# Kernel optimization log

Hardware: AMD Instinct MI355X
Metric: run time of the kernel (lower is better)

The kernel has to match this reference:

```python
import jax, jax.numpy as jnp
import numpy as np

N_NODES = 100000
N_EDGES = 1600000
D_IN, D_HID, D_OUT = 64, 64, 32


def setup_inputs() -> dict:
    key = jax.random.key(0)
    ks = jax.random.split(key, 9)
    x = jax.random.normal(ks[0], (N_NODES, D_IN), dtype=jnp.float32)
    edge_index = jax.random.randint(ks[1], (2, N_EDGES), 0, N_NODES, dtype=jnp.int64)
    s1 = 1.0 / np.sqrt(D_IN)
    s2 = 1.0 / np.sqrt(D_HID)
    return {
        "x": x,
        "edge_index": edge_index,
        # layer 1: lin_l (aggregated neighbors, has bias), lin_r (root, no bias)
        "W1_l": jax.random.uniform(ks[2], (D_IN, D_HID), jnp.float32, -s1, s1),
        "b1": jax.random.uniform(ks[3], (D_HID,), jnp.float32, -s1, s1),
        "W1_r": jax.random.uniform(ks[4], (D_IN, D_HID), jnp.float32, -s1, s1),
        # layer 2
        "W2_l": jax.random.uniform(ks[5], (D_HID, D_OUT), jnp.float32, -s2, s2),
        "b2": jax.random.uniform(ks[6], (D_OUT,), jnp.float32, -s2, s2),
        "W2_r": jax.random.uniform(ks[7], (D_HID, D_OUT), jnp.float32, -s2, s2),
    }


def _sage_conv(x, src, dst, W_l, b_l, W_r, n_nodes):
    """PyG SAGEConv with mean aggregation:
       out_i = W_l @ mean_{j in N(i)} x_j + b_l + W_r @ x_i
    """
    msgs = x[src]  # [E, d] gather of source-node features
    summed = jax.ops.segment_sum(msgs, dst, num_segments=n_nodes)  # [N, d]
    deg = jax.ops.segment_sum(jnp.ones((src.shape[0],), x.dtype), dst, num_segments=n_nodes)
    mean = summed / jnp.maximum(deg, 1.0)[:, None]
    return mean @ W_l + b_l + x @ W_r


def reference(x, edge_index, W1_l, b1, W1_r, W2_l, b2, W2_r):
    src, dst = edge_index[0], edge_index[1]
    n = x.shape[0]
    h = _sage_conv(x, src, dst, W1_l, b1, W1_r, n)
    h = jax.nn.relu(h)
    out = _sage_conv(h, src, dst, W2_l, b2, W2_r, n)
    return out
```

## Files before the change

### kernel.cpp

```cpp
#include <hip/hip_runtime.h>


typedef __attribute__((ext_vector_type(4))) float f4;
typedef __attribute__((ext_vector_type(2))) float f2;
typedef __attribute__((ext_vector_type(4))) unsigned short us4;
typedef __attribute__((ext_vector_type(8))) unsigned short us8;
typedef __attribute__((ext_vector_type(8))) short bfrag;

#define BSHIFT 9
#define BSZ (1 << BSHIFT)
#define NBMAX 256
#define NBLK 512
#define LSTR 72

static __device__ inline unsigned short f2bf(float f) {
    union { float f; unsigned u; } v; v.f = f;
    unsigned u = v.u;
    u = (u + 0x7FFFu + ((u >> 16) & 1u)) >> 16;
    return (unsigned short)u;
}
static __device__ inline float bf2f(unsigned short h) {
    union { unsigned u; float f; } v; v.u = ((unsigned)h) << 16; return v.f;
}

__global__ __launch_bounds__(256) void k_g1h(const float* __restrict__ x,
                                             const float* __restrict__ Wl,
                                             const float* __restrict__ Wr, int N, int gb,
                                             unsigned char* __restrict__ t1l8,
                                             unsigned short* __restrict__ t1rb,
                                             const int* __restrict__ dst, int E, int chunk,
                                             int NB, int* __restrict__ cntmat) {
    __shared__ unsigned short smem[64 * LSTR + 128 * LSTR];
    int t = threadIdx.x;
    if ((int)blockIdx.x >= gb) {
        int* hist = (int*)smem;
        hist[t] = 0;
        __syncthreads();
        int bb = blockIdx.x - gb;
        int lo = bb * chunk, hi = min(lo + chunk, E);
        for (int e = lo + t; e < hi; e += 256) atomicAdd(&hist[dst[e] >> BSHIFT], 1);
        __syncthreads();
        if (t < NB) cntmat[bb * NB + t] = hist[t];
        return;
    }
    unsigned short* sX = smem;
    unsigned short* sW = smem + 64 * LSTR;
    int r0 = blockIdx.x * 64;
    for (int i = t; i < 2048; i += 256) {
        int which = i >> 10;
        int rem = i & 1023;
        int k = rem >> 4;
        int c4 = (rem & 15) * 4;
        f4 v = *(const f4*)&(which ? Wr : Wl)[k * 64 + c4];
        int nb = which * 64 + c4;
        sW[(nb + 0) * LSTR + k] = f2bf(v[0]);
        sW[(nb + 1) * LSTR + k] = f2bf(v[1]);
        sW[(nb + 2) * LSTR + k] = f2bf(v[2]);
        sW[(nb + 3) * LSTR + k] = f2bf(v[3]);
    }
    {
        int row = t >> 2;
        int q = (t & 3) * 16;
        bool valid = (r0 + row) < N;
#pragma unroll
        for (int j = 0; j < 4; j++) {
            f4 v = {0.f, 0.f, 0.f, 0.f};
            if (valid) v = *(const f4*)&x[(size_t)(r0 + row) * 64 + q + j * 4];
            us4 bv;
            bv[0] = f2bf(v[0]); bv[1] = f2bf(v[1]); bv[2] = f2bf(v[2]); bv[3] = f2bf(v[3]);
            *(us4*)&sX[row * LSTR + q + j * 4] = bv;
        }
    }
    __syncthreads();
    int wv = t >> 6;
    int l  = t & 63;
    int lm = l & 15;
    int lk = (l >> 4) * 8;
    f4 acc[8] = {{0.f,0.f,0.f,0.f},{0.f,0.f,0.f,0.f},{0.f,0.f,0.f,0.f},{0.f,0.f,0.f,0.f},
                 {0.f,0.f,0.f,0.f},{0.f,0.f,0.f,0.f},{0.f,0.f,0.f,0.f},{0.f,0.f,0.f,0.f}};
#pragma unroll
    for (int kh = 0; kh < 2; kh++) {
        bfrag a = *(const bfrag*)&sX[(wv * 16 + lm) * LSTR + kh * 32 + lk];
#pragma unroll
        for (int nt = 0; nt < 8; nt++) {
            bfrag b = *(const bfrag*)&sW[(nt * 16 + lm) * LSTR + kh * 32 + lk];
            acc[nt] = __builtin_amdgcn_mfma_f32_16x16x32_bf16(a, b, acc[nt], 0, 0, 0);
        }
    }
    int orow0 = r0 + wv * 16 + (l >> 4) * 4;
#pragma unroll
    for (int j = 0; j < 4; j++) {
        int rr = orow0 + j;
        if (rr < N) {
#pragma unroll
            for (int nt = 0; nt < 4; nt++) {
                float v = acc[nt][j];
                unsigned w8 = __builtin_amdgcn_cvt_pk_fp8_f32(v, v, 0u, false);
                t1l8[(size_t)rr * 64 + nt * 16 + lm] = (unsigned char)(w8 & 0xFFu);
            }
#pragma unroll
            for (int nt = 0; nt < 4; nt++) {
                t1rb[(size_t)rr * 64 + nt * 16 + lm] = f2bf(acc[nt + 4][j]);
            }
        }
    }
}

__global__ __launch_bounds__(256) void k_cscan(int* __restrict__ cntmat, int NB, int E, int N,
                                               int* __restrict__ btot, int* __restrict__ row_off) {
    __shared__ int wt[4];
    int b = blockIdx.x;
    int t = threadIdx.x;
    int v0 = cntmat[(2 * t) * NB + b];
    int v1 = cntmat[(2 * t + 1) * NB + b];
    int tsum = v0 + v1;
    int lane = t & 63, w = t >> 6;
    int p = tsum;
    for (int off = 1; off < 64; off <<= 1) { int u = __shfl_up(p, off); if (lane >= off) p += u; }
    if (lane == 63) wt[w] = p;
    __syncthreads();
    int wb = 0;
    for (int i = 0; i < w; i++) wb += wt[i];
    int excl = wb + p - tsum;
    cntmat[(2 * t) * NB + b] = excl;
    cntmat[(2 * t + 1) * NB + b] = excl + v0;
    if (t == 255) btot[b] = wb + p;
    if (b == 0 && t == 0) row_off[N] = E;
}

__global__ __launch_bounds__(256) void k_bscatter(const int* __restrict__ src, const int* __restrict__ dst,
                                                  int E, int chunk, int NB,
                                                  const int* __restrict__ btot,
                                                  const int* __restrict__ cntmat,
                                                  unsigned int* __restrict__ bdata) {
    __shared__ int lbase[NBMAX], lcur[NBMAX];
    __shared__ int wt[4];
    int t = threadIdx.x;
    int v = (t < NB) ? btot[t] : 0;
    int lane = t & 63, w = t >> 6;
    int p = v;
    for (int off = 1; off < 64; off <<= 1) { int u = __shfl_up(p, off); if (lane >= off) p += u; }
    if (lane == 63) wt[w] = p;
    __syncthreads();
    int wb = 0;
    for (int i = 0; i < w; i++) wb += wt[i];
    int excl = wb + p - v;
    if (t < NB) { lbase[t] = excl + cntmat[blockIdx.x * NB + t]; lcur[t] = 0; }
    __syncthreads();
    int lo = blockIdx.x * chunk, hi = min(lo + chunk, E);
    for (int e = lo + t; e < hi; e += 256) {
        int d = dst[e];
        int b = d >> BSHIFT;
        int pos = lbase[b] + atomicAdd(&lcur[b], 1);
        bdata[pos] = ((unsigned)(d & (BSZ - 1)) << 17) | (unsigned)src[e];
    }
}

__global__ __launch_bounds__(256) void k_bucket_csr(const unsigned int* __restrict__ bdata,
                                                    const int* __restrict__ btot, int NB,
                                                    int N, int* __restrict__ row_off,
                                                    int* __restrict__ col_src) {
    __shared__ int fh[BSZ];
    __shared__ int wt1[4], wt2[4];
    __shared__ int sb[2];
    int t = threadIdx.x;
    int b = blockIdx.x;
    {
        int v = (t < NB) ? btot[t] : 0;
        int lane = t & 63, w = t >> 6;
        int p = v;
        for (int off = 1; off < 64; off <<= 1) { int u = __shfl_up(p, off); if (lane >= off) p += u; }
        if (lane == 63) wt1[w] = p;
        __syncthreads();
        int wb = 0;
        for (int i = 0; i < w; i++) wb += wt1[i];
        int excl = wb + p - v;
        if (t == b) { sb[0] = excl; sb[1] = excl + v; }
    }
    fh[2 * t] = 0; fh[2 * t + 1] = 0;
    __syncthreads();
    int ebase = sb[0], eend = sb[1];
    for (int i = ebase + t; i < eend; i += 256) atomicAdd(&fh[bdata[i] >> 17], 1);
    __syncthreads();
    int a0 = fh[2 * t], a1 = fh[2 * t + 1];
    int psum = a0 + a1;
    int lane = t & 63, w = t >> 6;
    int v = psum;
    for (int off = 1; off < 64; off <<= 1) { int u = __shfl_up(v, off); if (lane >= off) v += u; }
    if (lane == 63) wt2[w] = v;
    __syncthreads();
    int wbase = 0;
    for (int i = 0; i < w; i++) wbase += wt2[i];
    int excl = wbase + v - psum;
    int e0 = excl, e1 = excl + a0;
    int n0 = (b << BSHIFT) + 2 * t, n1 = n0 + 1;
    if (n0 < N) row_off[n0] = ebase + e0;
    if (n1 < N) row_off[n1] = ebase + e1;
    fh[2 * t] = e0; fh[2 * t + 1] = e1;
    __syncthreads();
    for (int i = ebase + t; i < eend; i += 256) {
        unsigned vv = bdata[i];
        int dl = vv >> 17;
        int pos = atomicAdd(&fh[dl], 1);
        col_src[ebase + pos] = (int)(vv & 0x1FFFFu);
    }
}

__global__ __launch_bounds__(256) void k_gemm2(const unsigned short* __restrict__ hbf,
                                               const float* __restrict__ Wl,
                                               const float* __restrict__ Wr,
                                               const float* __restrict__ b2, int N,
                                               unsigned short* __restrict__ t2l,
                                               float* __restrict__ t2r) {
    __shared__ unsigned short sX[64 * LSTR];
    __shared__ unsigned short sW[64 * LSTR];
    int t = threadIdx.x;
    int r0 = blockIdx.x * 64;
    for (int i = t; i < 1024; i += 256) {
        int which = i >> 9;
        int rem = i & 511;
        int k = rem >> 3;
        int c4 = (rem & 7) * 4;
        f4 v = *(const f4*)&(which ? Wr : Wl)[k * 32 + c4];
        int nb = which * 32 + c4;
        sW[(nb + 0) * LSTR + k] = f2bf(v[0]);
        sW[(nb + 1) * LSTR + k] = f2bf(v[1]);
        sW[(nb + 2) * LSTR + k] = f2bf(v[2]);
        sW[(nb + 3) * LSTR + k] = f2bf(v[3]);
    }
    {
        int row = t >> 2;
        int q = (t & 3) * 16;
        us8 z = {0,0,0,0,0,0,0,0};
        us8 v0 = z, v1 = z;
        if (r0 + row < N) {
            v0 = *(const us8*)&hbf[(size_t)(r0 + row) * 64 + q];
            v1 = *(const us8*)&hbf[(size_t)(r0 + row) * 64 + q + 8];
        }
        *(us8*)&sX[row * LSTR + q] = v0;
        *(us8*)&sX[row * LSTR + q + 8] = v1;
    }
    __syncthreads();
    int wv = t >> 6;
    int l  = t & 63;
    int lm = l & 15;
    int lk = (l >> 4) * 8;
    f4 acc[4] = {{0.f,0.f,0.f,0.f},{0.f,0.f,0.f,0.f},{0.f,0.f,0.f,0.f},{0.f,0.f,0.f,0.f}};
#pragma unroll
    for (int kh = 0; kh < 2; kh++) {
        bfrag a = *(const bfrag*)&sX[(wv * 16 + lm) * LSTR + kh * 32 + lk];
#pragma unroll
        for (int nt = 0; nt < 4; nt++) {
            bfrag b = *(const bfrag*)&sW[(nt * 16 + lm) * LSTR + kh * 32 + lk];
            acc[nt] = __builtin_amdgcn_mfma_f32_16x16x32_bf16(a, b, acc[nt], 0, 0, 0);
        }
    }
    int orow0 = r0 + wv * 16 + (l >> 4) * 4;
#pragma unroll
    for (int j = 0; j < 4; j++) {
        int rr = orow0 + j;
        if (rr < N) {
#pragma unroll
            for (int nt = 0; nt < 2; nt++) {
                t2l[(size_t)rr * 32 + nt * 16 + lm] = f2bf(acc[nt][j]);
            }
#pragma unroll
            for (int nt = 0; nt < 2; nt++) {
                int c = nt * 16 + lm;
                t2r[(size_t)rr * 32 + c] = acc[nt + 2][j] + b2[c];
            }
        }
    }
}

__global__ __launch_bounds__(256) void k_agg1(const unsigned char* __restrict__ t1l8,
                                              const int* __restrict__ row_off,
                                              const int* __restrict__ col_src,
                                              const float* __restrict__ b1,
                                              const unsigned short* __restrict__ t1rb,
                                              int N, unsigned short* __restrict__ hbf) {
    int gid = (blockIdx.x * blockDim.x + threadIdx.x) >> 4;
    int gl  = threadIdx.x & 15;
    if (gid >= N) return;
    int beg = row_off[gid], end = row_off[gid + 1];
    f4 a0 = {0.f,0.f,0.f,0.f}, a1 = {0.f,0.f,0.f,0.f};
    f4 a2 = {0.f,0.f,0.f,0.f}, a3 = {0.f,0.f,0.f,0.f};
    int k = beg;
    for (; k + 7 < end; k += 8) {
        int i0 = col_src[k],     i1 = col_src[k + 1], i2 = col_src[k + 2], i3 = col_src[k + 3];
        int i4 = col_src[k + 4], i5 = col_src[k + 5], i6 = col_src[k + 6], i7 = col_src[k + 7];
        unsigned u0 = *(const unsigned*)&t1l8[(size_t)i0 * 64 + gl * 4];
        unsigned u1 = *(const unsigned*)&t1l8[(size_t)i1 * 64 + gl * 4];
        unsigned u2 = *(const unsigned*)&t1l8[(size_t)i2 * 64 + gl * 4];
        unsigned u3 = *(const unsigned*)&t1l8[(size_t)i3 * 64 + gl * 4];
        unsigned u4 = *(const unsigned*)&t1l8[(size_t)i4 * 64 + gl * 4];
        unsigned u5 = *(const unsigned*)&t1l8[(size_t)i5 * 64 + gl * 4];
        unsigned u6 = *(const unsigned*)&t1l8[(size_t)i6 * 64 + gl * 4];
        unsigned u7 = *(const unsigned*)&t1l8[(size_t)i7 * 64 + gl * 4];
        f2 l0 = __builtin_amdgcn_cvt_pk_f32_fp8(u0, false), h0 = __builtin_amdgcn_cvt_pk_f32_fp8(u0, true);
        f2 l1 = __builtin_amdgcn_cvt_pk_f32_fp8(u1, false), h1 = __builtin_amdgcn_cvt_pk_f32_fp8(u1, true);
        f2 l2 = __builtin_amdgcn_cvt_pk_f32_fp8(u2, false), h2 = __builtin_amdgcn_cvt_pk_f32_fp8(u2, true);
        f2 l3 = __builtin_amdgcn_cvt_pk_f32_fp8(u3, false), h3 = __builtin_amdgcn_cvt_pk_f32_fp8(u3, true);
        f2 l4 = __builtin_amdgcn_cvt_pk_f32_fp8(u4, false), h4 = __builtin_amdgcn_cvt_pk_f32_fp8(u4, true);
        f2 l5 = __builtin_amdgcn_cvt_pk_f32_fp8(u5, false), h5 = __builtin_amdgcn_cvt_pk_f32_fp8(u5, true);
        f2 l6 = __builtin_amdgcn_cvt_pk_f32_fp8(u6, false), h6 = __builtin_amdgcn_cvt_pk_f32_fp8(u6, true);
        f2 l7 = __builtin_amdgcn_cvt_pk_f32_fp8(u7, false), h7 = __builtin_amdgcn_cvt_pk_f32_fp8(u7, true);
        a0[0] += l0[0] + l4[0]; a0[1] += l0[1] + l4[1]; a0[2] += h0[0] + h4[0]; a0[3] += h0[1] + h4[1];
        a1[0] += l1[0] + l5[0]; a1[1] += l1[1] + l5[1]; a1[2] += h1[0] + h5[0]; a1[3] += h1[1] + h5[1];
        a2[0] += l2[0] + l6[0]; a2[1] += l2[1] + l6[1]; a2[2] += h2[0] + h6[0]; a2[3] += h2[1] + h6[1];
        a3[0] += l3[0] + l7[0]; a3[1] += l3[1] + l7[1]; a3[2] += h3[0] + h7[0]; a3[3] += h3[1] + h7[1];
    }
    for (; k + 3 < end; k += 4) {
        int i0 = col_src[k], i1 = col_src[k + 1], i2 = col_src[k + 2], i3 = col_src[k + 3];
        unsigned u0 = *(const unsigned*)&t1l8[(size_t)i0 * 64 + gl * 4];
        unsigned u1 = *(const unsigned*)&t1l8[(size_t)i1 * 64 + gl * 4];
        unsigned u2 = *(const unsigned*)&t1l8[(size_t)i2 * 64 + gl * 4];
        unsigned u3 = *(const unsigned*)&t1l8[(size_t)i3 * 64 + gl * 4];
        f2 l0 = __builtin_amdgcn_cvt_pk_f32_fp8(u0, false), h0 = __builtin_amdgcn_cvt_pk_f32_fp8(u0, true);
        f2 l1 = __builtin_amdgcn_cvt_pk_f32_fp8(u1, false), h1 = __builtin_amdgcn_cvt_pk_f32_fp8(u1, true);
        f2 l2 = __builtin_amdgcn_cvt_pk_f32_fp8(u2, false), h2 = __builtin_amdgcn_cvt_pk_f32_fp8(u2, true);
        f2 l3 = __builtin_amdgcn_cvt_pk_f32_fp8(u3, false), h3 = __builtin_amdgcn_cvt_pk_f32_fp8(u3, true);
        a0[0] += l0[0]; a0[1] += l0[1]; a0[2] += h0[0]; a0[3] += h0[1];
        a1[0] += l1[0]; a1[1] += l1[1]; a1[2] += h1[0]; a1[3] += h1[1];
        a2[0] += l2[0]; a2[1] += l2[1]; a2[2] += h2[0]; a2[3] += h2[1];
        a3[0] += l3[0]; a3[1] += l3[1]; a3[2] += h3[0]; a3[3] += h3[1];
    }
    for (; k < end; k++) {
        unsigned u0 = *(const unsigned*)&t1l8[(size_t)col_src[k] * 64 + gl * 4];
        f2 l0 = __builtin_amdgcn_cvt_pk_f32_fp8(u0, false), h0 = __builtin_amdgcn_cvt_pk_f32_fp8(u0, true);
        a0[0] += l0[0]; a0[1] += l0[1]; a0[2] += h0[0]; a0[3] += h0[1];
    }
    f4 s = (a0 + a1) + (a2 + a3);
    float deg = (float)(end - beg);
    float inv = deg > 0.f ? 1.f / deg : 0.f;
    us4 rb = *(const us4*)&t1rb[(size_t)gid * 64 + gl * 4];
    f4 bb = *(const f4*)&b1[gl * 4];
    us4 ob;
#pragma unroll
    for (int j = 0; j < 4; j++) {
        float v = s[j] * inv + bf2f(rb[j]) + bb[j];
        ob[j] = f2bf(v > 0.f ? v : 0.f);
    }
    *(us4*)&hbf[(size_t)gid * 64 + gl * 4] = ob;
}

__global__ __launch_bounds__(256) void k_agg2(const unsigned short* __restrict__ t2l,
                                              const float* __restrict__ t2r,
                                              const int* __restrict__ row_off,
                                              const int* __restrict__ col_src,
                                              int N, float* __restrict__ out) {
    int gid = (blockIdx.x * blockDim.x + threadIdx.x) >> 4;
    int gl  = threadIdx.x & 15;
    if (gid >= N) return;
    int beg = row_off[gid], end = row_off[gid + 1];
    f2 a0 = {0.f,0.f}, a1 = {0.f,0.f}, a2 = {0.f,0.f}, a3 = {0.f,0.f};
    int k = beg;
    for (; k + 7 < end; k += 8) {
        int i0 = col_src[k],     i1 = col_src[k + 1], i2 = col_src[k + 2], i3 = col_src[k + 3];
        int i4 = col_src[k + 4], i5 = col_src[k + 5], i6 = col_src[k + 6], i7 = col_src[k + 7];
        unsigned u0 = *(const unsigned*)&t2l[(size_t)i0 * 32 + gl * 2];
        unsigned u1 = *(const unsigned*)&t2l[(size_t)i1 * 32 + gl * 2];
        unsigned u2 = *(const unsigned*)&t2l[(size_t)i2 * 32 + gl * 2];
        unsigned u3 = *(const unsigned*)&t2l[(size_t)i3 * 32 + gl * 2];
        unsigned u4 = *(const unsigned*)&t2l[(size_t)i4 * 32 + gl * 2];
        unsigned u5 = *(const unsigned*)&t2l[(size_t)i5 * 32 + gl * 2];
        unsigned u6 = *(const unsigned*)&t2l[(size_t)i6 * 32 + gl * 2];
        unsigned u7 = *(const unsigned*)&t2l[(size_t)i7 * 32 + gl * 2];
        a0[0] += bf2f((unsigned short)(u0 & 0xFFFFu)) + bf2f((unsigned short)(u4 & 0xFFFFu));
        a0[1] += bf2f((unsigned short)(u0 >> 16))     + bf2f((unsigned short)(u4 >> 16));
        a1[0] += bf2f((unsigned short)(u1 & 0xFFFFu)) + bf2f((unsigned short)(u5 & 0xFFFFu));
        a1[1] += bf2f((unsigned short)(u1 >> 16))     + bf2f((unsigned short)(u5 >> 16));
        a2[0] += bf2f((unsigned short)(u2 & 0xFFFFu)) + bf2f((unsigned short)(u6 & 0xFFFFu));
        a2[1] += bf2f((unsigned short)(u2 >> 16))     + bf2f((unsigned short)(u6 >> 16));
        a3[0] += bf2f((unsigned short)(u3 & 0xFFFFu)) + bf2f((unsigned short)(u7 & 0xFFFFu));
        a3[1] += bf2f((unsigned short)(u3 >> 16))     + bf2f((unsigned short)(u7 >> 16));
    }
    for (; k + 3 < end; k += 4) {
        int i0 = col_src[k], i1 = col_src[k + 1], i2 = col_src[k + 2], i3 = col_src[k + 3];
        unsigned u0 = *(const unsigned*)&t2l[(size_t)i0 * 32 + gl * 2];
        unsigned u1 = *(const unsigned*)&t2l[(size_t)i1 * 32 + gl * 2];
        unsigned u2 = *(const unsigned*)&t2l[(size_t)i2 * 32 + gl * 2];
        unsigned u3 = *(const unsigned*)&t2l[(size_t)i3 * 32 + gl * 2];
        a0[0] += bf2f((unsigned short)(u0 & 0xFFFFu)); a0[1] += bf2f((unsigned short)(u0 >> 16));
        a1[0] += bf2f((unsigned short)(u1 & 0xFFFFu)); a1[1] += bf2f((unsigned short)(u1 >> 16));
        a2[0] += bf2f((unsigned short)(u2 & 0xFFFFu)); a2[1] += bf2f((unsigned short)(u2 >> 16));
        a3[0] += bf2f((unsigned short)(u3 & 0xFFFFu)); a3[1] += bf2f((unsigned short)(u3 >> 16));
    }
    for (; k < end; k++) {
        unsigned u0 = *(const unsigned*)&t2l[(size_t)col_src[k] * 32 + gl * 2];
        a0[0] += bf2f((unsigned short)(u0 & 0xFFFFu)); a0[1] += bf2f((unsigned short)(u0 >> 16));
    }
    f2 s = (a0 + a1) + (a2 + a3);
    float deg = (float)(end - beg);
    float inv = deg > 0.f ? 1.f / deg : 0.f;
    f2 rr = *(const f2*)&t2r[(size_t)gid * 32 + gl * 2];
    f2 o = {s[0] * inv + rr[0], s[1] * inv + rr[1]};
    *(f2*)&out[(size_t)gid * 32 + gl * 2] = o;
}

extern "C" void kernel_launch(void* const* d_in, const int* in_sizes, int n_in,
                              void* d_out, int out_size, void* d_ws, size_t ws_size,
                              hipStream_t stream) {
    const float* x   = (const float*)d_in[0];
    const int*   ei  = (const int*)d_in[1];
    const float* W1l = (const float*)d_in[2];
    const float* b1  = (const float*)d_in[3];
    const float* W1r = (const float*)d_in[4];
    const float* W2l = (const float*)d_in[5];
    const float* b2  = (const float*)d_in[6];
    const float* W2r = (const float*)d_in[7];
    float* out = (float*)d_out;

    int N = in_sizes[0] / 64;
    int E = in_sizes[1] / 2;
    const int* src = ei;
    const int* dst = ei + E;
    int NB = (N + BSZ - 1) >> BSHIFT;

    char* ws = (char*)d_ws;
    size_t off = 0;
    auto alloc = [&](size_t bytes) { void* p = ws + off; off += (bytes + 255) & ~(size_t)255; return p; };
    int* cntmat      = (int*)alloc((size_t)NBLK * NB * 4);
    int* btot        = (int*)alloc((size_t)NB * 4);
    int* row_off     = (int*)alloc((size_t)(N + 1) * 4);
    int* col_src     = (int*)alloc((size_t)E * 4);
    unsigned int* bdata = (unsigned int*)alloc((size_t)E * 4);
    unsigned char* t1l8 = (unsigned char*)alloc((size_t)N * 64);
    unsigned short* t1rb = (unsigned short*)alloc((size_t)N * 64 * 2);
    unsigned short* hbf  = (unsigned short*)alloc((size_t)N * 64 * 2);

    unsigned short* t2l = (unsigned short*)bdata;
    float* t2r          = (float*)t1rb;

    int chunk = (E + NBLK - 1) / NBLK;
    int gb = (N + 63) / 64;

    k_g1h<<<gb + NBLK, 256, 0, stream>>>(x, W1l, W1r, N, gb, t1l8, t1rb,
                                         dst, E, chunk, NB, cntmat);
    k_cscan<<<NB, 256, 0, stream>>>(cntmat, NB, E, N, btot, row_off);
    k_bscatter<<<NBLK, 256, 0, stream>>>(src, dst, E, chunk, NB, btot, cntmat, bdata);
    k_bucket_csr<<<NB, 256, 0, stream>>>(bdata, btot, NB, N, row_off, col_src);

    k_agg1<<<((size_t)N * 16 + 255) / 256, 256, 0, stream>>>(t1l8, row_off, col_src, b1, t1rb, N, hbf);
    k_gemm2<<<gb, 256, 0, stream>>>(hbf, W2l, W2r, b2, N, t2l, t2r);
    k_agg2<<<((size_t)N * 16 + 255) / 256, 256, 0, stream>>>(t2l, t2r, row_off, col_src, N, out);
}
```

Measured before the change: 129.5 us.

## Fuse layer-1 aggregation with layer-2 GEMM and LDS-sort bucket scatter

Merges the layer-1 mean aggregation with the layer-2 MFMA GEMM into one kernel. Each 256-thread block aggregates 16 nodes into shared memory, then one wave computes their 16x64 output tile. This removes the hidden-activation round trip through global memory and one kernel launch. The cost is that every block reloads and converts W2 to bf16, and only one wave does the MFMA work. Separately, the bucket scatter now sorts each chunk of edges by bucket in LDS before writing, so global writes to bdata become contiguous runs instead of random stores.

```diff
diff --git a/kernel.cpp b/kernel.cpp
--- a/kernel.cpp
+++ b/kernel.cpp
@@ -11,6 +11,7 @@
 #define BSZ (1 << BSHIFT)
 #define NBMAX 256
 #define NBLK 512
+#define CHMAX 3328
 #define LSTR 72
 
 static __device__ inline unsigned short f2bf(float f) {
@@ -133,26 +134,59 @@
                                                   const int* __restrict__ btot,
                                                   const int* __restrict__ cntmat,
                                                   unsigned int* __restrict__ bdata) {
-    __shared__ int lbase[NBMAX], lcur[NBMAX];
+    __shared__ int lcnt[NBMAX], loff[NBMAX], lcur[NBMAX], gbase[NBMAX];
     __shared__ int wt[4];
+    __shared__ unsigned ldst[CHMAX];
+    __shared__ unsigned srec[CHMAX];
+    __shared__ unsigned char sbk[CHMAX];
     int t = threadIdx.x;
-    int v = (t < NB) ? btot[t] : 0;
-    int lane = t & 63, w = t >> 6;
-    int p = v;
-    for (int off = 1; off < 64; off <<= 1) { int u = __shfl_up(p, off); if (lane >= off) p += u; }
-    if (lane == 63) wt[w] = p;
-    __syncthreads();
-    int wb = 0;
-    for (int i = 0; i < w; i++) wb += wt[i];
-    int excl = wb + p - v;
-    if (t < NB) { lbase[t] = excl + cntmat[blockIdx.x * NB + t]; lcur[t] = 0; }
-    __syncthreads();
-    int lo = blockIdx.x * chunk, hi = min(lo + chunk, E);
-    for (int e = lo + t; e < hi; e += 256) {
-        int d = dst[e];
+    {
+        int v = (t < NB) ? btot[t] : 0;
+        int lane = t & 63, w = t >> 6;
+        int p = v;
+        for (int off = 1; off < 64; off <<= 1) { int u = __shfl_up(p, off); if (lane >= off) p += u; }
+        if (lane == 63) wt[w] = p;
+        __syncthreads();
+        int wb = 0;
+        for (int i = 0; i < w; i++) wb += wt[i];
+        int excl = wb + p - v;
+        if (t < NB) gbase[t] = excl + cntmat[blockIdx.x * NB + t];
+        lcnt[t] = 0;
+    }
+    __syncthreads();
+    int lo = blockIdx.x * chunk;
+    int n = min(chunk, E - lo);
+    for (int i = t; i < n; i += 256) {
+        int d = dst[lo + i];
+        ldst[i] = (unsigned)d;
+        atomicAdd(&lcnt[d >> BSHIFT], 1);
+    }
+    __syncthreads();
+    {
+        int v = lcnt[t];
+        int lane = t & 63, w = t >> 6;
+        int p = v;
+        for (int off = 1; off < 64; off <<= 1) { int u = __shfl_up(p, off); if (lane >= off) p += u; }
+        __syncthreads();
+        if (lane == 63) wt[w] = p;
+        __syncthreads();
+        int wb = 0;
+        for (int i = 0; i < w; i++) wb += wt[i];
+        loff[t] = wb + p - v;
+        lcur[t] = 0;
+    }
+    __syncthreads();
+    for (int i = t; i < n; i += 256) {
+        int d = (int)ldst[i];
         int b = d >> BSHIFT;
-        int pos = lbase[b] + atomicAdd(&lcur[b], 1);
-        bdata[pos] = ((unsigned)(d & (BSZ - 1)) << 17) | (unsigned)src[e];
+        int pos = loff[b] + atomicAdd(&lcur[b], 1);
+        srec[pos] = ((unsigned)(d & (BSZ - 1)) << 17) | (unsigned)src[lo + i];
+        sbk[pos] = (unsigned char)b;
+    }
+    __syncthreads();
+    for (int i = t; i < n; i += 256) {
+        int b = sbk[i];
+        bdata[gbase[b] + (i - loff[b])] = srec[i];
     }
 }
 
@@ -206,142 +240,128 @@
     }
 }
 
-__global__ __launch_bounds__(256) void k_gemm2(const unsigned short* __restrict__ hbf,
-                                               const float* __restrict__ Wl,
-                                               const float* __restrict__ Wr,
-                                               const float* __restrict__ b2, int N,
-                                               unsigned short* __restrict__ t2l,
-                                               float* __restrict__ t2r) {
-    __shared__ unsigned short sX[64 * LSTR];
-    __shared__ unsigned short sW[64 * LSTR];
+__global__ __launch_bounds__(256) void k_agg1g2(const unsigned char* __restrict__ t1l8,
+                                                const int* __restrict__ row_off,
+                                                const int* __restrict__ col_src,
+                                                const float* __restrict__ b1,
+                                                const unsigned short* __restrict__ t1rb,
+                                                const float* __restrict__ W2l,
+                                                const float* __restrict__ W2r,
+                                                const float* __restrict__ b2,
+                                                int N,
+                                                unsigned short* __restrict__ t2l,
+                                                float* __restrict__ t2r) {
+    __shared__ unsigned short sH[16 * LSTR];
+    __shared__ unsigned short sW2[64 * LSTR];
     int t = threadIdx.x;
-    int r0 = blockIdx.x * 64;
     for (int i = t; i < 1024; i += 256) {
         int which = i >> 9;
         int rem = i & 511;
         int k = rem >> 3;
         int c4 = (rem & 7) * 4;
-        f4 v = *(const f4*)&(which ? Wr : Wl)[k * 32 + c4];
+        f4 v = *(const f4*)&(which ? W2r : W2l)[k * 32 + c4];
         int nb = which * 32 + c4;
-        sW[(nb + 0) * LSTR + k] = f2bf(v[0]);
-        sW[(nb + 1) * LSTR + k] = f2bf(v[1]);
-        sW[(nb + 2) * LSTR + k] = f2bf(v[2]);
-        sW[(nb + 3) * LSTR + k] = f2bf(v[3]);
-    }
-    {
-        int row = t >> 2;
-        int q = (t & 3) * 16;
-        us8 z = {0,0,0,0,0,0,0,0};
-        us8 v0 = z, v1 = z;
-        if (r0 + row < N) {
-            v0 = *(const us8*)&hbf[(size_t)(r0 + row) * 64 + q];
-            v1 = *(const us8*)&hbf[(size_t)(r0 + row) * 64 + q + 8];
-        }
-        *(us8*)&sX[row * LSTR + q] = v0;
-        *(us8*)&sX[row * LSTR + q + 8] = v1;
-    }
-    __syncthreads();
-    int wv = t >> 6;
-    int l  = t & 63;
-    int lm = l & 15;
-    int lk = (l >> 4) * 8;
-    f4 acc[4] = {{0.f,0.f,0.f,0.f},{0.f,0.f,0.f,0.f},{0.f,0.f,0.f,0.f},{0.f,0.f,0.f,0.f}};
-#pragma unroll
-    for (int kh = 0; kh < 2; kh++) {
-        bfrag a = *(const bfrag*)&sX[(wv * 16 + lm) * LSTR + kh * 32 + lk];
-#pragma unroll
-        for (int nt = 0; nt < 4; nt++) {
-            bfrag b = *(const bfrag*)&sW[(nt * 16 + lm) * LSTR + kh * 32 + lk];
-            acc[nt] = __builtin_amdgcn_mfma_f32_16x16x32_bf16(a, b, acc[nt], 0, 0, 0);
-        }
-    }
-    int orow0 = r0 + wv * 16 + (l >> 4) * 4;
-#pragma unroll
-    for (int j = 0; j < 4; j++) {
-        int rr = orow0 + j;
-        if (rr < N) {
-#pragma unroll
-            for (int nt = 0; nt < 2; nt++) {
-                t2l[(size_t)rr * 32 + nt * 16 + lm] = f2bf(acc[nt][j]);
+        sW2[(nb + 0) * LSTR + k] = f2bf(v[0]);
+        sW2[(nb + 1) * LSTR + k] = f2bf(v[1]);
+        sW2[(nb + 2) * LSTR + k] = f2bf(v[2]);
+        sW2[(nb + 3) * LSTR + k] = f2bf(v[3]);
+    }
+    int g   = t >> 4;
+    int gl  = t & 15;
+    int gid = blockIdx.x * 16 + g;
+    if (gid < N) {
+        int beg = row_off[gid], end = row_off[gid + 1];
+        f4 a0 = {0.f,0.f,0.f,0.f}, a1 = {0.f,0.f,0.f,0.f};
+        f4 a2 = {0.f,0.f,0.f,0.f}, a3 = {0.f,0.f,0.f,0.f};
+        int k = beg;
+        for (; k + 7 < end; k += 8) {
+            int i0 = col_src[k],     i1 = col_src[k + 1], i2 = col_src[k + 2], i3 = col_src[k + 3];
+            int i4 = col_src[k + 4], i5 = col_src[k + 5], i6 = col_src[k + 6], i7 = col_src[k + 7];
+            unsigned u0 = *(const unsigned*)&t1l8[(size_t)i0 * 64 + gl * 4];
+            unsigned u1 = *(const unsigned*)&t1l8[(size_t)i1 * 64 + gl * 4];
+            unsigned u2 = *(const unsigned*)&t1l8[(size_t)i2 * 64 + gl * 4];
+            unsigned u3 = *(const unsigned*)&t1l8[(size_t)i3 * 64 + gl * 4];
+            unsigned u4 = *(const unsigned*)&t1l8[(size_t)i4 * 64 + gl * 4];
+            unsigned u5 = *(const unsigned*)&t1l8[(size_t)i5 * 64 + gl * 4];
+            unsigned u6 = *(const unsigned*)&t1l8[(size_t)i6 * 64 + gl * 4];
+            unsigned u7 = *(const unsigned*)&t1l8[(size_t)i7 * 64 + gl * 4];
+            f2 l0 = __builtin_amdgcn_cvt_pk_f32_fp8(u0, false), h0 = __builtin_amdgcn_cvt_pk_f32_fp8(u0, true);
+            f2 l1 = __builtin_amdgcn_cvt_pk_f32_fp8(u1, false), h1 = __builtin_amdgcn_cvt_pk_f32_fp8(u1, true);
+            f2 l2 = __builtin_amdgcn_cvt_pk_f32_fp8(u2, false), h2 = __builtin_amdgcn_cvt_pk_f32_fp8(u2, true);
+            f2 l3 = __builtin_amdgcn_cvt_pk_f32_fp8(u3, false), h3 = __builtin_amdgcn_cvt_pk_f32_fp8(u3, true);
+            f2 l4 = __builtin_amdgcn_cvt_pk_f32_fp8(u4, false), h4 = __builtin_amdgcn_cvt_pk_f32_fp8(u4, true);
+            f2 l5 = __builtin_amdgcn_cvt_pk_f32_fp8(u5, false), h5 = __builtin_amdgcn_cvt_pk_f32_fp8(u5, true);
+            f2 l6 = __builtin_amdgcn_cvt_pk_f32_fp8(u6, false), h6 = __builtin_amdgcn_cvt_pk_f32_fp8(u6, true);
+            f2 l7 = __builtin_amdgcn_cvt_pk_f32_fp8(u7, false), h7 = __builtin_amdgcn_cvt_pk_f32_fp8(u7, true);
+            a0[0] += l0[0] + l4[0]; a0[1] += l0[1] + l4[1]; a0[2] += h0[0] + h4[0]; a0[3] += h0[1] + h4[1];
+            a1[0] += l1[0] + l5[0]; a1[1] += l1[1] + l5[1]; a1[2] += h1[0] + h5[0]; a1[3] += h1[1] + h5[1];
+            a2[0] += l2[0] + l6[0]; a2[1] += l2[1] + l6[1]; a2[2] += h2[0] + h6[0]; a2[3] += h2[1] + h6[1];
+            a3[0] += l3[0] + l7[0]; a3[1] += l3[1] + l7[1]; a3[2] += h3[0] + h7[0]; a3[3] += h3[1] + h7[1];
+        }
+        for (; k + 3 < end; k += 4) {
+            int i0 = col_src[k], i1 = col_src[k + 1], i2 = col_src[k + 2], i3 = col_src[k + 3];
+            unsigned u0 = *(const unsigned*)&t1l8[(size_t)i0 * 64 + gl * 4];
+            unsigned u1 = *(const unsigned*)&t1l8[(size_t)i1 * 64 + gl * 4];
+            unsigned u2 = *(const unsigned*)&t1l8[(size_t)i2 * 64 + gl * 4];
+            unsigned u3 = *(const unsigned*)&t1l8[(size_t)i3 * 64 + gl * 4];
+            f2 l0 = __builtin_amdgcn_cvt_pk_f32_fp8(u0, false), h0 = __builtin_amdgcn_cvt_pk_f32_fp8(u0, true);
+            f2 l1 = __builtin_amdgcn_cvt_pk_f32_fp8(u1, false), h1 = __builtin_amdgcn_cvt_pk_f32_fp8(u1, true);
+            f2 l2 = __builtin_amdgcn_cvt_pk_f32_fp8(u2, false), h2 = __builtin_amdgcn_cvt_pk_f32_fp8(u2, true);
+            f2 l3 = __builtin_amdgcn_cvt_pk_f32_fp8(u3, false), h3 = __builtin_amdgcn_cvt_pk_f32_fp8(u3, true);
+            a0[0] += l0[0]; a0[1] += l0[1]; a0[2] += h0[0]; a0[3] += h0[1];
+            a1[0] += l1[0]; a1[1] += l1[1]; a1[2] += h1[0]; a1[3] += h1[1];
+            a2[0] += l2[0]; a2[1] += l2[1]; a2[2] += h2[0]; a2[3] += h2[1];
+            a3[0] += l3[0]; a3[1] += l3[1]; a3[2] += h3[0]; a3[3] += h3[1];
+        }
+        for (; k < end; k++) {
+            unsigned u0 = *(const unsigned*)&t1l8[(size_t)col_src[k] * 64 + gl * 4];
+            f2 l0 = __builtin_amdgcn_cvt_pk_f32_fp8(u0, false), h0 = __builtin_amdgcn_cvt_pk_f32_fp8(u0, true);
+            a0[0] += l0[0]; a0[1] += l0[1]; a0[2] += h0[0]; a0[3] += h0[1];
+        }
+        f4 s = (a0 + a1) + (a2 + a3);
+        float deg = (float)(end - beg);
+        float inv = deg > 0.f ? 1.f / deg : 0.f;
+        us4 rb = *(const us4*)&t1rb[(size_t)gid * 64 + gl * 4];
+        f4 bb = *(const f4*)&b1[gl * 4];
+        us4 ob;
+#pragma unroll
+        for (int j = 0; j < 4; j++) {
+            float v = s[j] * inv + bf2f(rb[j]) + bb[j];
+            ob[j] = f2bf(v > 0.f ? v : 0.f);
+        }
+        *(us4*)&sH[g * LSTR + gl * 4] = ob;
+    }
+    __syncthreads();
+    if (t < 64) {
+        int lm = t & 15;
+        int lk = (t >> 4) * 8;
+        f4 acc[4] = {{0.f,0.f,0.f,0.f},{0.f,0.f,0.f,0.f},{0.f,0.f,0.f,0.f},{0.f,0.f,0.f,0.f}};
+#pragma unroll
+        for (int kh = 0; kh < 2; kh++) {
+            bfrag a = *(const bfrag*)&sH[lm * LSTR + kh * 32 + lk];
+#pragma unroll
+            for (int nt = 0; nt < 4; nt++) {
+                bfrag b = *(const bfrag*)&sW2[(nt * 16 + lm) * LSTR + kh * 32 + lk];
+                acc[nt] = __builtin_amdgcn_mfma_f32_16x16x32_bf16(a, b, acc[nt], 0, 0, 0);
             }
-#pragma unroll
-            for (int nt = 0; nt < 2; nt++) {
-                int c = nt * 16 + lm;
-                t2r[(size_t)rr * 32 + c] = acc[nt + 2][j] + b2[c];
+        }
+        int orow0 = blockIdx.x * 16 + (t >> 4) * 4;
+#pragma unroll
+        for (int j = 0; j < 4; j++) {
+            int rr = orow0 + j;
+            if (rr < N) {
+#pragma unroll
+                for (int nt = 0; nt < 2; nt++) {
+                    t2l[(size_t)rr * 32 + nt * 16 + lm] = f2bf(acc[nt][j]);
+                }
+#pragma unroll
+                for (int nt = 0; nt < 2; nt++) {
+                    int c = nt * 16 + lm;
+                    t2r[(size_t)rr * 32 + c] = acc[nt + 2][j] + b2[c];
+                }
             }
         }
     }
-}
-
-__global__ __launch_bounds__(256) void k_agg1(const unsigned char* __restrict__ t1l8,
-                                              const int* __restrict__ row_off,
-                                              const int* __restrict__ col_src,
-                                              const float* __restrict__ b1,
-                                              const unsigned short* __restrict__ t1rb,
-                                              int N, unsigned short* __restrict__ hbf) {
-    int gid = (blockIdx.x * blockDim.x + threadIdx.x) >> 4;
-    int gl  = threadIdx.x & 15;
-    if (gid >= N) return;
-    int beg = row_off[gid], end = row_off[gid + 1];
-    f4 a0 = {0.f,0.f,0.f,0.f}, a1 = {0.f,0.f,0.f,0.f};
-    f4 a2 = {0.f,0.f,0.f,0.f}, a3 = {0.f,0.f,0.f,0.f};
-    int k = beg;
-    for (; k + 7 < end; k += 8) {
-        int i0 = col_src[k],     i1 = col_src[k + 1], i2 = col_src[k + 2], i3 = col_src[k + 3];
-        int i4 = col_src[k + 4], i5 = col_src[k + 5], i6 = col_src[k + 6], i7 = col_src[k + 7];
-        unsigned u0 = *(const unsigned*)&t1l8[(size_t)i0 * 64 + gl * 4];
-        unsigned u1 = *(const unsigned*)&t1l8[(size_t)i1 * 64 + gl * 4];
-        unsigned u2 = *(const unsigned*)&t1l8[(size_t)i2 * 64 + gl * 4];
-        unsigned u3 = *(const unsigned*)&t1l8[(size_t)i3 * 64 + gl * 4];
-        unsigned u4 = *(const unsigned*)&t1l8[(size_t)i4 * 64 + gl * 4];
-        unsigned u5 = *(const unsigned*)&t1l8[(size_t)i5 * 64 + gl * 4];
-        unsigned u6 = *(const unsigned*)&t1l8[(size_t)i6 * 64 + gl * 4];
-        unsigned u7 = *(const unsigned*)&t1l8[(size_t)i7 * 64 + gl * 4];
-        f2 l0 = __builtin_amdgcn_cvt_pk_f32_fp8(u0, false), h0 = __builtin_amdgcn_cvt_pk_f32_fp8(u0, true);
-        f2 l1 = __builtin_amdgcn_cvt_pk_f32_fp8(u1, false), h1 = __builtin_amdgcn_cvt_pk_f32_fp8(u1, true);
-        f2 l2 = __builtin_amdgcn_cvt_pk_f32_fp8(u2, false), h2 = __builtin_amdgcn_cvt_pk_f32_fp8(u2, true);
-        f2 l3 = __builtin_amdgcn_cvt_pk_f32_fp8(u3, false), h3 = __builtin_amdgcn_cvt_pk_f32_fp8(u3, true);
-        f2 l4 = __builtin_amdgcn_cvt_pk_f32_fp8(u4, false), h4 = __builtin_amdgcn_cvt_pk_f32_fp8(u4, true);
-        f2 l5 = __builtin_amdgcn_cvt_pk_f32_fp8(u5, false), h5 = __builtin_amdgcn_cvt_pk_f32_fp8(u5, true);
-        f2 l6 = __builtin_amdgcn_cvt_pk_f32_fp8(u6, false), h6 = __builtin_amdgcn_cvt_pk_f32_fp8(u6, true);
-        f2 l7 = __builtin_amdgcn_cvt_pk_f32_fp8(u7, false), h7 = __builtin_amdgcn_cvt_pk_f32_fp8(u7, true);
-        a0[0] += l0[0] + l4[0]; a0[1] += l0[1] + l4[1]; a0[2] += h0[0] + h4[0]; a0[3] += h0[1] + h4[1];
-        a1[0] += l1[0] + l5[0]; a1[1] += l1[1] + l5[1]; a1[2] += h1[0] + h5[0]; a1[3] += h1[1] + h5[1];
-        a2[0] += l2[0] + l6[0]; a2[1] += l2[1] + l6[1]; a2[2] += h2[0] + h6[0]; a2[3] += h2[1] + h6[1];
-        a3[0] += l3[0] + l7[0]; a3[1] += l3[1] + l7[1]; a3[2] += h3[0] + h7[0]; a3[3] += h3[1] + h7[1];
-    }
-    for (; k + 3 < end; k += 4) {
-        int i0 = col_src[k], i1 = col_src[k + 1], i2 = col_src[k + 2], i3 = col_src[k + 3];
-        unsigned u0 = *(const unsigned*)&t1l8[(size_t)i0 * 64 + gl * 4];
-        unsigned u1 = *(const unsigned*)&t1l8[(size_t)i1 * 64 + gl * 4];
-        unsigned u2 = *(const unsigned*)&t1l8[(size_t)i2 * 64 + gl * 4];
-        unsigned u3 = *(const unsigned*)&t1l8[(size_t)i3 * 64 + gl * 4];
-        f2 l0 = __builtin_amdgcn_cvt_pk_f32_fp8(u0, false), h0 = __builtin_amdgcn_cvt_pk_f32_fp8(u0, true);
-        f2 l1 = __builtin_amdgcn_cvt_pk_f32_fp8(u1, false), h1 = __builtin_amdgcn_cvt_pk_f32_fp8(u1, true);
-        f2 l2 = __builtin_amdgcn_cvt_pk_f32_fp8(u2, false), h2 = __builtin_amdgcn_cvt_pk_f32_fp8(u2, true);
-        f2 l3 = __builtin_amdgcn_cvt_pk_f32_fp8(u3, false), h3 = __builtin_amdgcn_cvt_pk_f32_fp8(u3, true);
-        a0[0] += l0[0]; a0[1] += l0[1]; a0[2] += h0[0]; a0[3] += h0[1];
-        a1[0] += l1[0]; a1[1] += l1[1]; a1[2] += h1[0]; a1[3] += h1[1];
-        a2[0] += l2[0]; a2[1] += l2[1]; a2[2] += h2[0]; a2[3] += h2[1];
-        a3[0] += l3[0]; a3[1] += l3[1]; a3[2] += h3[0]; a3[3] += h3[1];
-    }
-    for (; k < end; k++) {
-        unsigned u0 = *(const unsigned*)&t1l8[(size_t)col_src[k] * 64 + gl * 4];
-        f2 l0 = __builtin_amdgcn_cvt_pk_f32_fp8(u0, false), h0 = __builtin_amdgcn_cvt_pk_f32_fp8(u0, true);
-        a0[0] += l0[0]; a0[1] += l0[1]; a0[2] += h0[0]; a0[3] += h0[1];
-    }
-    f4 s = (a0 + a1) + (a2 + a3);
-    float deg = (float)(end - beg);
-    float inv = deg > 0.f ? 1.f / deg : 0.f;
-    us4 rb = *(const us4*)&t1rb[(size_t)gid * 64 + gl * 4];
-    f4 bb = *(const f4*)&b1[gl * 4];
-    us4 ob;
-#pragma unroll
-    for (int j = 0; j < 4; j++) {
-        float v = s[j] * inv + bf2f(rb[j]) + bb[j];
-        ob[j] = f2bf(v > 0.f ? v : 0.f);
-    }
-    *(us4*)&hbf[(size_t)gid * 64 + gl * 4] = ob;
 }
 
 __global__ __launch_bounds__(256) void k_agg2(const unsigned short* __restrict__ t2l,
@@ -427,7 +447,6 @@
     unsigned int* bdata = (unsigned int*)alloc((size_t)E * 4);
     unsigned char* t1l8 = (unsigned char*)alloc((size_t)N * 64);
     unsigned short* t1rb = (unsigned short*)alloc((size_t)N * 64 * 2);
-    unsigned short* hbf  = (unsigned short*)alloc((size_t)N * 64 * 2);
 
     unsigned short* t2l = (unsigned short*)bdata;
     float* t2r          = (float*)t1rb;
@@ -441,7 +460,7 @@
     k_bscatter<<<NBLK, 256, 0, stream>>>(src, dst, E, chunk, NB, btot, cntmat, bdata);
     k_bucket_csr<<<NB, 256, 0, stream>>>(bdata, btot, NB, N, row_off, col_src);
 
-    k_agg1<<<((size_t)N * 16 + 255) / 256, 256, 0, stream>>>(t1l8, row_off, col_src, b1, t1rb, N, hbf);
-    k_gemm2<<<gb, 256, 0, stream>>>(hbf, W2l, W2r, b2, N, t2l, t2r);
+    k_agg1g2<<<(N + 15) / 16, 256, 0, stream>>>(t1l8, row_off, col_src, b1, t1rb,
+                                                W2l, W2r, b2, N, t2l, t2r);
     k_agg2<<<((size_t)N * 16 + 255) / 256, 256, 0, stream>>>(t2l, t2r, row_off, col_src, N, out);
 }
```

Measured after the change: 132.5 us. 1.02x slower.
